# Optimization experiments

Hardware: AMD Instinct MI355X
Metric: run time of the kernel (lower is better)

The kernel has to match this reference:

```python
import jax, jax.numpy as jnp
import numpy as np

STATE = 1024

def setup_inputs() -> dict:
    key = jax.random.key(0)
    k1, k2, k3, k4, k5 = jax.random.split(key, 5)
    B, IN, S = 4096, 1024, STATE
    stdv = 1.0 / np.sqrt(S)
    return {
        "input": jax.random.normal(k1, (B, IN), jnp.float32),
        "old_h": jax.random.normal(k2, (B, S), jnp.float32),
        "old_cell": jax.random.normal(k3, (B, S), jnp.float32),
        "weights": jax.random.uniform(k4, (4 * S, IN + S), jnp.float32, -stdv, stdv),
        "bias": jax.random.uniform(k5, (4 * S,), jnp.float32, -stdv, stdv),
    }

def reference(input, old_h, old_cell, weights, bias):
    # Fused gate GEMM: X = [input, old_h] -> [B, IN+S]; gates -> [B, 4S]
    X = jnp.concatenate([input, old_h], axis=1)
    gates = X @ weights.T + bias
    f, i, o, g = jnp.split(gates, 4, axis=1)
    f = jax.nn.sigmoid(f)
    i = jax.nn.sigmoid(i)
    o = jax.nn.sigmoid(o)
    g = jnp.tanh(g)
    new_cell = f * old_cell + i * g
    new_h = o * jnp.tanh(new_cell)
    return new_h, new_cell
```

## Files before the change

kernel.cpp:

```cpp
#include <hip/hip_runtime.h>
#include <stdint.h>

#define NB   4096
#define KD   2048
#define ND   4096
#define SD   1024

#define BM   256
#define BN   256
#define BK   64
#define NKT  (KD / BK)

using f32x4  = __attribute__((ext_vector_type(4))) float;
using bf16x8 = __attribute__((ext_vector_type(8))) short;

typedef const __attribute__((address_space(1))) uint32_t* gas_u32;
typedef __attribute__((address_space(3))) uint32_t* las_u32;

__device__ __forceinline__ unsigned short f2bf(float f) {
    union { float f; uint32_t u; } c; c.f = f;
    uint32_t u = c.u;
    uint32_t r = (u + 0x7fffu + ((u >> 16) & 1u)) >> 16;
    return (unsigned short)r;
}

__device__ __forceinline__ void async_load16(const void* gsrc, void* ldst) {
    __builtin_amdgcn_global_load_lds((gas_u32)gsrc, (las_u32)ldst, 16, 0, 0);
}

__device__ __forceinline__ float frcp(float x) { return __builtin_amdgcn_rcpf(x); }
__device__ __forceinline__ float sigm(float x) { return frcp(1.f + __expf(-x)); }
__device__ __forceinline__ float tanh_fast(float x) {
    return 1.f - 2.f * frcp(1.f + __expf(2.f * x));
}

__global__ void pack_kernel(const float* __restrict__ input,
                            const float* __restrict__ old_h,
                            const float* __restrict__ weights,
                            const float* __restrict__ bias,
                            unsigned short* __restrict__ Xb,
                            unsigned short* __restrict__ Wb,
                            float* __restrict__ biasR) {
    const int XCH = NB * (KD / 4);
    const int WCH = ND * (KD / 4);
    const int BCH = ND / 4;
    const int total = XCH + WCH + BCH;
    for (int c = blockIdx.x * blockDim.x + threadIdx.x; c < total;
         c += gridDim.x * blockDim.x) {
        if (c < XCH) {
            int b  = c >> 9;
            int k  = (c & 511) << 2;
            const float* src = (k < 1024) ? (input + (size_t)b * 1024 + k)
                                          : (old_h + (size_t)b * 1024 + (k - 1024));
            float4 v = *reinterpret_cast<const float4*>(src);
            ushort4 o;
            o.x = f2bf(v.x); o.y = f2bf(v.y); o.z = f2bf(v.z); o.w = f2bf(v.w);
            *reinterpret_cast<ushort4*>(Xb + (size_t)b * KD + k) = o;
        } else if (c < XCH + WCH) {
            int cc = c - XCH;
            int n  = cc >> 9;
            int k  = (cc & 511) << 2;
            int srow = ((n >> 4) & 3) * SD + ((n >> 6) * 16 + (n & 15));
            float4 v = *reinterpret_cast<const float4*>(weights + (size_t)srow * KD + k);
            ushort4 o;
            o.x = f2bf(v.x); o.y = f2bf(v.y); o.z = f2bf(v.z); o.w = f2bf(v.w);
            *reinterpret_cast<ushort4*>(Wb + (size_t)n * KD + k) = o;
        } else {
            int n4 = (c - XCH - WCH) << 2;
            #pragma unroll
            for (int t = 0; t < 4; ++t) {
                int n = n4 + t;
                biasR[n] = bias[((n >> 4) & 3) * SD + ((n >> 6) * 16 + (n & 15))];
            }
        }
    }
}

#define SEG(DB, AB, HALF) (((((DB) * 2 + (AB)) * 2) + (HALF)) * 8192)

#define SBAR   __builtin_amdgcn_s_barrier()
#define SFENCE __builtin_amdgcn_sched_barrier(0)
#define ASM_LGKM0  asm volatile("s_waitcnt lgkmcnt(0)" ::: "memory")
#define ASM_VMCNT2 asm volatile("s_waitcnt vmcnt(2)" ::: "memory")
#define ASM_VMCNT4 asm volatile("s_waitcnt vmcnt(4)" ::: "memory")

__launch_bounds__(512, 2)
__global__ void lstm_gemm(const unsigned short* __restrict__ Xb,
                          const unsigned short* __restrict__ Wb,
                          const float* __restrict__ biasR,
                          const float* __restrict__ old_cell,
                          float* __restrict__ new_h,
                          float* __restrict__ new_cell) {
    __shared__ unsigned short lds[65536];

    const int tid  = threadIdx.x;
    const int lane = tid & 63;
    const int wid  = tid >> 6;
    const int wm   = wid >> 2;
    const int wn   = wid & 3;
    const int l15  = lane & 15;
    const int krow = lane >> 4;

    const int wg    = blockIdx.x;
    const int swz   = (wg & 7) * 32 + (wg >> 3);
    const int mblk  = swz >> 4;
    const int nblk  = swz & 15;
    const int rbase = mblk * BM;
    const int nbase = nblk * BN;

    const int c0 = tid, c1 = tid + 512;
    const int srow0 = c0 >> 3, sk0 = ((c0 & 7) ^ (srow0 & 7)) * 8;
    const int srow1 = c1 >> 3, sk1 = ((c1 & 7) ^ (srow1 & 7)) * 8;

    f32x4  acc[8][4] = {};
    bf16x8 a[4][2];
    bf16x8 bm[2][2];
    bf16x8 ba[2][2];

#define STAGE(PTR, TB, KT, DB, AB, HALF) do {                                   \
        async_load16((PTR) + (size_t)((TB) + (HALF) * 128 + srow0) * KD +       \
                         (KT) * BK + sk0,                                       \
                     lds + SEG(DB, AB, HALF) + c0 * 8);                         \
        async_load16((PTR) + (size_t)((TB) + (HALF) * 128 + srow1) * KD +       \
                         (KT) * BK + sk1,                                       \
                     lds + SEG(DB, AB, HALF) + c1 * 8);                         \
    } while (0)

#define LOAD_A(DB, MQ) do {                                                     \
        const unsigned short* base_ = lds + SEG(DB, 0, 0) + wm * 8192;          \
        _Pragma("unroll") for (int i_ = 0; i_ < 4; ++i_)                        \
        _Pragma("unroll") for (int kk_ = 0; kk_ < 2; ++kk_) {                   \
            int r_ = (MQ) * 64 + i_ * 16 + l15;                                 \
            int s_ = kk_ * 4 + krow;                                            \
            a[i_][kk_] = *reinterpret_cast<const bf16x8*>(                      \
                base_ + r_ * 64 + ((s_ ^ (r_ & 7)) * 8));                       \
        }                                                                       \
    } while (0)

#define LOAD_B_TO(DST, DB, NQ) do {                                             \
        const unsigned short* base_ = lds + SEG(DB, 1, 0) + (wn >> 1) * 8192;   \
        _Pragma("unroll") for (int j_ = 0; j_ < 2; ++j_)                        \
        _Pragma("unroll") for (int kk_ = 0; kk_ < 2; ++kk_) {                   \
            int r_ = (wn & 1) * 64 + ((NQ) * 2 + j_) * 16 + l15;                \
            int s_ = kk_ * 4 + krow;                                            \
            DST[j_][kk_] = *reinterpret_cast<const bf16x8*>(                    \
                base_ + r_ * 64 + ((s_ ^ (r_ & 7)) * 8));                       \
        }                                                                       \
    } while (0)

#define MMA_Q(MQ, NQH, BB) do {                                                 \
        _Pragma("unroll") for (int i_ = 0; i_ < 4; ++i_)                        \
        _Pragma("unroll") for (int j_ = 0; j_ < 2; ++j_)                        \
        _Pragma("unroll") for (int kk_ = 0; kk_ < 2; ++kk_)                     \
            acc[(MQ) * 4 + i_][(NQH) * 2 + j_] =                                \
                __builtin_amdgcn_mfma_f32_16x16x32_bf16(                        \
                    a[i_][kk_], BB[j_][kk_],                                    \
                    acc[(MQ) * 4 + i_][(NQH) * 2 + j_], 0, 0, 0);               \
    } while (0)

#define PH_HEAD   SFENCE; SBAR; ASM_LGKM0; SFENCE; __builtin_amdgcn_s_setprio(1)
#define PH_HEADV  SFENCE; ASM_VMCNT2; SBAR; ASM_LGKM0; SFENCE; __builtin_amdgcn_s_setprio(1)
#define PH_TAIL   __builtin_amdgcn_s_setprio(0); SFENCE; SBAR; SFENCE

    STAGE(Wb, nbase, 0, 0, 1, 0);
    STAGE(Wb, nbase, 0, 0, 1, 1);
    STAGE(Xb, rbase, 0, 0, 0, 0);
    STAGE(Xb, rbase, 0, 0, 0, 1);
    STAGE(Wb, nbase, 1, 1, 1, 0);
    STAGE(Wb, nbase, 1, 1, 1, 1);
    ASM_VMCNT4;
    SBAR; SFENCE;
    LOAD_B_TO(bm, 0, 0);
    LOAD_A(0, 0);

#define KBODY(TT, BUF) do {                                                     \
        const int kt1_ = ((TT) + 1) & (NKT - 1);                                \
        const int kt2_ = ((TT) + 2) & (NKT - 1);                                \
        STAGE(Xb, rbase, kt1_, (BUF) ^ 1, 0, 0);                                \
        PH_HEAD;  MMA_Q(0, 0, bm); LOAD_B_TO(ba, BUF, 1);      PH_TAIL;         \
        STAGE(Xb, rbase, kt1_, (BUF) ^ 1, 0, 1);                                \
        PH_HEAD;  MMA_Q(0, 1, ba); LOAD_A(BUF, 1);             PH_TAIL;         \
        STAGE(Wb, nbase, kt2_, BUF, 1, 0);                                      \
        PH_HEADV; MMA_Q(1, 0, bm); LOAD_B_TO(bm, (BUF) ^ 1, 0); PH_TAIL;        \
        STAGE(Wb, nbase, kt2_, BUF, 1, 1);                                      \
        PH_HEAD;  MMA_Q(1, 1, ba); LOAD_A((BUF) ^ 1, 0);       PH_TAIL;         \
    } while (0)

    for (int t = 0; t < NKT; t += 2) {
        KBODY(t, 0);
        KBODY(t + 1, 1);
    }

    const int s = (nblk * 4 + wn) * 16 + l15;
    float bg[4];
    #pragma unroll
    for (int jj = 0; jj < 4; ++jj)
        bg[jj] = biasR[nbase + wn * 64 + jj * 16 + l15];

    #pragma unroll
    for (int mi = 0; mi < 8; ++mi) {
        #pragma unroll
        for (int r = 0; r < 4; ++r) {
            const int row = rbase + wm * 128 + mi * 16 + krow * 4 + r;
            float fg = sigm(acc[mi][0][r] + bg[0]);
            float ig = sigm(acc[mi][1][r] + bg[1]);
            float og = sigm(acc[mi][2][r] + bg[2]);
            float gg = tanh_fast(acc[mi][3][r] + bg[3]);
            float oc = old_cell[(size_t)row * SD + s];
            float nc = fmaf(fg, oc, ig * gg);
            float nh = og * tanh_fast(nc);
            new_h[(size_t)row * SD + s]    = nh;
            new_cell[(size_t)row * SD + s] = nc;
        }
    }
}

extern "C" void kernel_launch(void* const* d_in, const int* in_sizes, int n_in,
                              void* d_out, int out_size, void* d_ws, size_t ws_size,
                              hipStream_t stream) {
    const float* input    = (const float*)d_in[0];
    const float* old_h    = (const float*)d_in[1];
    const float* old_cell = (const float*)d_in[2];
    const float* weights  = (const float*)d_in[3];
    const float* bias     = (const float*)d_in[4];

    unsigned short* Xb  = (unsigned short*)d_ws;
    unsigned short* Wb  = (unsigned short*)((char*)d_ws + (size_t)16777216);
    float*          bR  = (float*)((char*)d_ws + (size_t)33554432);

    float* out_h = (float*)d_out;
    float* out_c = out_h + (size_t)NB * SD;

    pack_kernel<<<2048, 256, 0, stream>>>(input, old_h, weights, bias, Xb, Wb, bR);
    lstm_gemm<<<(NB / BM) * (ND / BN), 512, 0, stream>>>(Xb, Wb, bR, old_cell,
                                                         out_h, out_c);
}
```

Baseline: 79.02 us.

## Restructure K-loop to load and consume LDS fragments per k-half phase

Replaces the register-prefetched fragment pipeline with per-phase loads that are used immediately. Each of the four phases now loads an A quarter for one k-half and, in the first two, a full B k-half, then issues 16 MFMAs. The explicit lgkmcnt waits and priority bumps are removed, and a single vmcnt wait is placed at the end of the body. This shrinks the fragment register footprint and simplifies synchronisation, but LDS read latency is no longer hidden behind the previous phase's MFMAs.

```diff
diff --git a/kernel.cpp b/kernel.cpp
--- a/kernel.cpp
+++ b/kernel.cpp
@@ -80,8 +80,6 @@
 
 #define SBAR   __builtin_amdgcn_s_barrier()
 #define SFENCE __builtin_amdgcn_sched_barrier(0)
-#define ASM_LGKM0  asm volatile("s_waitcnt lgkmcnt(0)" ::: "memory")
-#define ASM_VMCNT2 asm volatile("s_waitcnt vmcnt(2)" ::: "memory")
 #define ASM_VMCNT4 asm volatile("s_waitcnt vmcnt(4)" ::: "memory")
 
 __launch_bounds__(512, 2)
@@ -113,9 +111,9 @@
     const int srow1 = c1 >> 3, sk1 = ((c1 & 7) ^ (srow1 & 7)) * 8;
 
     f32x4  acc[8][4] = {};
-    bf16x8 a[4][2];
-    bf16x8 bm[2][2];
-    bf16x8 ba[2][2];
+    bf16x8 a[4];
+    bf16x8 bk0[4];
+    bf16x8 bk1[4];
 
 #define STAGE(PTR, TB, KT, DB, AB, HALF) do {                                   \
         async_load16((PTR) + (size_t)((TB) + (HALF) * 128 + srow0) * KD +       \
@@ -126,41 +124,33 @@
                      lds + SEG(DB, AB, HALF) + c1 * 8);                         \
     } while (0)
 
-#define LOAD_A(DB, MQ) do {                                                     \
+#define LOAD_A4(DB, MQ, KK) do {                                                \
         const unsigned short* base_ = lds + SEG(DB, 0, 0) + wm * 8192;          \
-        _Pragma("unroll") for (int i_ = 0; i_ < 4; ++i_)                        \
-        _Pragma("unroll") for (int kk_ = 0; kk_ < 2; ++kk_) {                   \
+        _Pragma("unroll") for (int i_ = 0; i_ < 4; ++i_) {                      \
             int r_ = (MQ) * 64 + i_ * 16 + l15;                                 \
-            int s_ = kk_ * 4 + krow;                                            \
-            a[i_][kk_] = *reinterpret_cast<const bf16x8*>(                      \
+            int s_ = (KK) * 4 + krow;                                           \
+            a[i_] = *reinterpret_cast<const bf16x8*>(                           \
                 base_ + r_ * 64 + ((s_ ^ (r_ & 7)) * 8));                       \
         }                                                                       \
     } while (0)
 
-#define LOAD_B_TO(DST, DB, NQ) do {                                             \
+#define LOAD_B4(DST, DB, KK) do {                                               \
         const unsigned short* base_ = lds + SEG(DB, 1, 0) + (wn >> 1) * 8192;   \
-        _Pragma("unroll") for (int j_ = 0; j_ < 2; ++j_)                        \
-        _Pragma("unroll") for (int kk_ = 0; kk_ < 2; ++kk_) {                   \
-            int r_ = (wn & 1) * 64 + ((NQ) * 2 + j_) * 16 + l15;                \
-            int s_ = kk_ * 4 + krow;                                            \
-            DST[j_][kk_] = *reinterpret_cast<const bf16x8*>(                    \
+        _Pragma("unroll") for (int j_ = 0; j_ < 4; ++j_) {                      \
+            int r_ = (wn & 1) * 64 + j_ * 16 + l15;                             \
+            int s_ = (KK) * 4 + krow;                                           \
+            DST[j_] = *reinterpret_cast<const bf16x8*>(                         \
                 base_ + r_ * 64 + ((s_ ^ (r_ & 7)) * 8));                       \
         }                                                                       \
     } while (0)
 
-#define MMA_Q(MQ, NQH, BB) do {                                                 \
+#define MMA16(MQ, BB) do {                                                      \
         _Pragma("unroll") for (int i_ = 0; i_ < 4; ++i_)                        \
-        _Pragma("unroll") for (int j_ = 0; j_ < 2; ++j_)                        \
-        _Pragma("unroll") for (int kk_ = 0; kk_ < 2; ++kk_)                     \
-            acc[(MQ) * 4 + i_][(NQH) * 2 + j_] =                                \
+        _Pragma("unroll") for (int j_ = 0; j_ < 4; ++j_)                        \
+            acc[(MQ) * 4 + i_][j_] =                                            \
                 __builtin_amdgcn_mfma_f32_16x16x32_bf16(                        \
-                    a[i_][kk_], BB[j_][kk_],                                    \
-                    acc[(MQ) * 4 + i_][(NQH) * 2 + j_], 0, 0, 0);               \
-    } while (0)
-
-#define PH_HEAD   SFENCE; SBAR; ASM_LGKM0; SFENCE; __builtin_amdgcn_s_setprio(1)
-#define PH_HEADV  SFENCE; ASM_VMCNT2; SBAR; ASM_LGKM0; SFENCE; __builtin_amdgcn_s_setprio(1)
-#define PH_TAIL   __builtin_amdgcn_s_setprio(0); SFENCE; SBAR; SFENCE
+                    a[i_], BB[j_], acc[(MQ) * 4 + i_][j_], 0, 0, 0);            \
+    } while (0)
 
     STAGE(Wb, nbase, 0, 0, 1, 0);
     STAGE(Wb, nbase, 0, 0, 1, 1);
@@ -169,21 +159,35 @@
     STAGE(Wb, nbase, 1, 1, 1, 0);
     STAGE(Wb, nbase, 1, 1, 1, 1);
     ASM_VMCNT4;
-    SBAR; SFENCE;
-    LOAD_B_TO(bm, 0, 0);
-    LOAD_A(0, 0);
+    SBAR;
+    SFENCE;
 
 #define KBODY(TT, BUF) do {                                                     \
         const int kt1_ = ((TT) + 1) & (NKT - 1);                                \
         const int kt2_ = ((TT) + 2) & (NKT - 1);                                \
+                      \
         STAGE(Xb, rbase, kt1_, (BUF) ^ 1, 0, 0);                                \
-        PH_HEAD;  MMA_Q(0, 0, bm); LOAD_B_TO(ba, BUF, 1);      PH_TAIL;         \
+        LOAD_A4(BUF, 0, 0);                                                     \
+        LOAD_B4(bk0, BUF, 0);                                                   \
+        MMA16(0, bk0);                                                          \
+        SBAR; SFENCE;                                                           \
+                      \
         STAGE(Xb, rbase, kt1_, (BUF) ^ 1, 0, 1);                                \
-        PH_HEAD;  MMA_Q(0, 1, ba); LOAD_A(BUF, 1);             PH_TAIL;         \
+        LOAD_A4(BUF, 0, 1);                                                     \
+        LOAD_B4(bk1, BUF, 1);                                                   \
+        MMA16(0, bk1);                                                          \
+        SBAR; SFENCE;                                                           \
+               \
         STAGE(Wb, nbase, kt2_, BUF, 1, 0);                                      \
-        PH_HEADV; MMA_Q(1, 0, bm); LOAD_B_TO(bm, (BUF) ^ 1, 0); PH_TAIL;        \
+        LOAD_A4(BUF, 1, 0);                                                     \
+        MMA16(1, bk0);                                                          \
+        SBAR; SFENCE;                                                           \
+              \
         STAGE(Wb, nbase, kt2_, BUF, 1, 1);                                      \
-        PH_HEAD;  MMA_Q(1, 1, ba); LOAD_A((BUF) ^ 1, 0);       PH_TAIL;         \
+        LOAD_A4(BUF, 1, 1);                                                     \
+        MMA16(1, bk1);                                                          \
+        ASM_VMCNT4;                                                             \
+        SBAR; SFENCE;                                                           \
     } while (0)
 
     for (int t = 0; t < NKT; t += 2) {
```

Result: no change. 77.80 us (-1.5%).

## Restructure GEMM main loop with precomputed LDS addresses and reordered load/MMA phases

Applied to the files above, without the earlier changes.

Rewrites the pipelined bf16 GEMM main loop. LDS read addresses are precomputed per lane as byte offsets, and global source pointers are hoisted. The LDS layout is changed into separate A and B regions. The phase schedule now issues LDS fragment loads before the MMAs, with partial lgkmcnt waits and explicit double-buffered B registers (b0/b1). The goal is to cut address arithmetic and improve overlap of LDS reads, async global loads and MFMA work. In exchange, it drops the sched_barrier fences and the memory clobbers on the lgkm waits, which risks compiler reordering and correctness or schedule problems.

```diff
diff --git a/kernel.cpp b/kernel.cpp
--- a/kernel.cpp
+++ b/kernel.cpp
@@ -76,13 +76,15 @@
     }
 }
 
-#define SEG(DB, AB, HALF) (((((DB) * 2 + (AB)) * 2) + (HALF)) * 8192)
+#define LDS_A(DB, HALF) (((DB) * 2 + (HALF)) * 16384)
+#define LDS_B(DB, HALF) (65536 + ((DB) * 2 + (HALF)) * 16384)
 
 #define SBAR   __builtin_amdgcn_s_barrier()
-#define SFENCE __builtin_amdgcn_sched_barrier(0)
-#define ASM_LGKM0  asm volatile("s_waitcnt lgkmcnt(0)" ::: "memory")
-#define ASM_VMCNT2 asm volatile("s_waitcnt vmcnt(2)" ::: "memory")
-#define ASM_VMCNT4 asm volatile("s_waitcnt vmcnt(4)" ::: "memory")
+#define LGKM8  asm volatile("s_waitcnt lgkmcnt(8)")
+#define LGKM0  asm volatile("s_waitcnt lgkmcnt(0)")
+#define VMC4   asm volatile("s_waitcnt vmcnt(4)" ::: "memory")
+#define PRIO1  __builtin_amdgcn_s_setprio(1)
+#define PRIO0  __builtin_amdgcn_s_setprio(0)
 
 __launch_bounds__(512, 2)
 __global__ void lstm_gemm(const unsigned short* __restrict__ Xb,
@@ -92,6 +94,7 @@
                           float* __restrict__ new_h,
                           float* __restrict__ new_cell) {
     __shared__ unsigned short lds[65536];
+    char* const ldsc = (char*)lds;
 
     const int tid  = threadIdx.x;
     const int lane = tid & 63;
@@ -108,43 +111,57 @@
     const int rbase = mblk * BM;
     const int nbase = nblk * BN;
 
+    const int lx   = l15 & 7;
+    const int lrow = l15 * 128;
+    const int sw0  = ((krow)     ^ lx) * 16;
+    const int sw1  = ((krow + 4) ^ lx) * 16;
+    const int vA00 = LDS_A(0, 0) + wm * 16384 + lrow + sw0;
+    const int vA01 = LDS_A(0, 0) + wm * 16384 + lrow + sw1;
+    const int vA10 = LDS_A(1, 0) + wm * 16384 + lrow + sw0;
+    const int vA11 = LDS_A(1, 0) + wm * 16384 + lrow + sw1;
+    const int bpan = (wn >> 1) * 16384 + (wn & 1) * 8192;
+    const int vB00 = LDS_B(0, 0) + bpan + lrow + sw0;
+    const int vB01 = LDS_B(0, 0) + bpan + lrow + sw1;
+    const int vB10 = LDS_B(1, 0) + bpan + lrow + sw0;
+    const int vB11 = LDS_B(1, 0) + bpan + lrow + sw1;
+
     const int c0 = tid, c1 = tid + 512;
     const int srow0 = c0 >> 3, sk0 = ((c0 & 7) ^ (srow0 & 7)) * 8;
     const int srow1 = c1 >> 3, sk1 = ((c1 & 7) ^ (srow1 & 7)) * 8;
+    const unsigned short* const pX0 = Xb + (size_t)(rbase + srow0) * KD + sk0;
+    const unsigned short* const pX1 = Xb + (size_t)(rbase + srow1) * KD + sk1;
+    const unsigned short* const pW0 = Wb + (size_t)(nbase + srow0) * KD + sk0;
+    const unsigned short* const pW1 = Wb + (size_t)(nbase + srow1) * KD + sk1;
+    const int ldst0 = tid * 16, ldst1 = tid * 16 + 8192;
 
     f32x4  acc[8][4] = {};
     bf16x8 a[4][2];
-    bf16x8 bm[2][2];
-    bf16x8 ba[2][2];
-
-#define STAGE(PTR, TB, KT, DB, AB, HALF) do {                                   \
-        async_load16((PTR) + (size_t)((TB) + (HALF) * 128 + srow0) * KD +       \
-                         (KT) * BK + sk0,                                       \
-                     lds + SEG(DB, AB, HALF) + c0 * 8);                         \
-        async_load16((PTR) + (size_t)((TB) + (HALF) * 128 + srow1) * KD +       \
-                         (KT) * BK + sk1,                                       \
-                     lds + SEG(DB, AB, HALF) + c1 * 8);                         \
-    } while (0)
-
-#define LOAD_A(DB, MQ) do {                                                     \
-        const unsigned short* base_ = lds + SEG(DB, 0, 0) + wm * 8192;          \
-        _Pragma("unroll") for (int i_ = 0; i_ < 4; ++i_)                        \
-        _Pragma("unroll") for (int kk_ = 0; kk_ < 2; ++kk_) {                   \
-            int r_ = (MQ) * 64 + i_ * 16 + l15;                                 \
-            int s_ = kk_ * 4 + krow;                                            \
-            a[i_][kk_] = *reinterpret_cast<const bf16x8*>(                      \
-                base_ + r_ * 64 + ((s_ ^ (r_ & 7)) * 8));                       \
+    bf16x8 b0[2][2];
+    bf16x8 b1[2][2];
+
+#define STAGE_X(KT, DB, HALF) do {                                              \
+        async_load16(pX0 + (HALF) * 128 * KD + (KT) * BK, ldsc + LDS_A(DB, HALF) + ldst0); \
+        async_load16(pX1 + (HALF) * 128 * KD + (KT) * BK, ldsc + LDS_A(DB, HALF) + ldst1); \
+    } while (0)
+#define STAGE_W(KT, DB, HALF) do {                                              \
+        async_load16(pW0 + (HALF) * 128 * KD + (KT) * BK, ldsc + LDS_B(DB, HALF) + ldst0); \
+        async_load16(pW1 + (HALF) * 128 * KD + (KT) * BK, ldsc + LDS_B(DB, HALF) + ldst1); \
+    } while (0)
+
+#define LOAD_A(V0, V1, MQ) do {                                                 \
+        _Pragma("unroll") for (int i_ = 0; i_ < 4; ++i_) {                      \
+            a[i_][0] = *reinterpret_cast<const bf16x8*>(                        \
+                ldsc + (V0) + (MQ) * 8192 + i_ * 2048);                         \
+            a[i_][1] = *reinterpret_cast<const bf16x8*>(                        \
+                ldsc + (V1) + (MQ) * 8192 + i_ * 2048);                         \
         }                                                                       \
     } while (0)
-
-#define LOAD_B_TO(DST, DB, NQ) do {                                             \
-        const unsigned short* base_ = lds + SEG(DB, 1, 0) + (wn >> 1) * 8192;   \
-        _Pragma("unroll") for (int j_ = 0; j_ < 2; ++j_)                        \
-        _Pragma("unroll") for (int kk_ = 0; kk_ < 2; ++kk_) {                   \
-            int r_ = (wn & 1) * 64 + ((NQ) * 2 + j_) * 16 + l15;                \
-            int s_ = kk_ * 4 + krow;                                            \
-            DST[j_][kk_] = *reinterpret_cast<const bf16x8*>(                    \
-                base_ + r_ * 64 + ((s_ ^ (r_ & 7)) * 8));                       \
+#define LOAD_B(DST, V0, V1, NQ) do {                                            \
+        _Pragma("unroll") for (int j_ = 0; j_ < 2; ++j_) {                      \
+            DST[j_][0] = *reinterpret_cast<const bf16x8*>(                      \
+                ldsc + (V0) + (NQ) * 4096 + j_ * 2048);                         \
+            DST[j_][1] = *reinterpret_cast<const bf16x8*>(                      \
+                ldsc + (V1) + (NQ) * 4096 + j_ * 2048);                         \
         }                                                                       \
     } while (0)
 
@@ -158,37 +175,46 @@
                     acc[(MQ) * 4 + i_][(NQH) * 2 + j_], 0, 0, 0);               \
     } while (0)
 
-#define PH_HEAD   SFENCE; SBAR; ASM_LGKM0; SFENCE; __builtin_amdgcn_s_setprio(1)
-#define PH_HEADV  SFENCE; ASM_VMCNT2; SBAR; ASM_LGKM0; SFENCE; __builtin_amdgcn_s_setprio(1)
-#define PH_TAIL   __builtin_amdgcn_s_setprio(0); SFENCE; SBAR; SFENCE
-
-    STAGE(Wb, nbase, 0, 0, 1, 0);
-    STAGE(Wb, nbase, 0, 0, 1, 1);
-    STAGE(Xb, rbase, 0, 0, 0, 0);
-    STAGE(Xb, rbase, 0, 0, 0, 1);
-    STAGE(Wb, nbase, 1, 1, 1, 0);
-    STAGE(Wb, nbase, 1, 1, 1, 1);
-    ASM_VMCNT4;
-    SBAR; SFENCE;
-    LOAD_B_TO(bm, 0, 0);
-    LOAD_A(0, 0);
-
-#define KBODY(TT, BUF) do {                                                     \
-        const int kt1_ = ((TT) + 1) & (NKT - 1);                                \
-        const int kt2_ = ((TT) + 2) & (NKT - 1);                                \
-        STAGE(Xb, rbase, kt1_, (BUF) ^ 1, 0, 0);                                \
-        PH_HEAD;  MMA_Q(0, 0, bm); LOAD_B_TO(ba, BUF, 1);      PH_TAIL;         \
-        STAGE(Xb, rbase, kt1_, (BUF) ^ 1, 0, 1);                                \
-        PH_HEAD;  MMA_Q(0, 1, ba); LOAD_A(BUF, 1);             PH_TAIL;         \
-        STAGE(Wb, nbase, kt2_, BUF, 1, 0);                                      \
-        PH_HEADV; MMA_Q(1, 0, bm); LOAD_B_TO(bm, (BUF) ^ 1, 0); PH_TAIL;        \
-        STAGE(Wb, nbase, kt2_, BUF, 1, 1);                                      \
-        PH_HEAD;  MMA_Q(1, 1, ba); LOAD_A((BUF) ^ 1, 0);       PH_TAIL;         \
-    } while (0)
+    STAGE_W(0, 0, 0);
+    STAGE_W(0, 0, 1);
+    STAGE_X(0, 0, 0);
+    STAGE_X(0, 0, 1);
+    STAGE_W(1, 1, 0);
+    STAGE_W(1, 1, 1);
+    VMC4;
+    SBAR;
 
     for (int t = 0; t < NKT; t += 2) {
-        KBODY(t, 0);
-        KBODY(t + 1, 1);
+        const int kt1 = t + 1;
+        const int kt2 = (t + 2) & (NKT - 1);
+        const int kt3 = (t + 3) & (NKT - 1);
+
+        LOAD_A(vA00, vA01, 0);
+        LOAD_B(b0, vB00, vB01, 0);
+        STAGE_X(kt1, 1, 0);
+        LGKM8;
+        SBAR; LGKM0; PRIO1; MMA_Q(0, 0, b0); PRIO0; SBAR;
+        LOAD_B(b1, vB00, vB01, 1);
+        STAGE_X(kt1, 1, 1);
+        SBAR; LGKM0; PRIO1; MMA_Q(0, 1, b1); PRIO0; SBAR;
+        LOAD_A(vA00, vA01, 1);
+        STAGE_W(kt2, 0, 0);
+        SBAR; LGKM0; PRIO1; MMA_Q(1, 0, b0); PRIO0; SBAR;
+        STAGE_W(kt2, 0, 1);
+        SBAR; LGKM0; PRIO1; MMA_Q(1, 1, b1); PRIO0; VMC4; SBAR;
+        LOAD_A(vA10, vA11, 0);
+        LOAD_B(b0, vB10, vB11, 0);
+        STAGE_X(kt2, 0, 0);
+        LGKM8;
+        SBAR; LGKM0; PRIO1; MMA_Q(0, 0, b0); PRIO0; SBAR;
+        LOAD_B(b1, vB10, vB11, 1);
+        STAGE_X(kt2, 0, 1);
+        SBAR; LGKM0; PRIO1; MMA_Q(0, 1, b1); PRIO0; SBAR;
+        LOAD_A(vA10, vA11, 1);
+        STAGE_W(kt3, 1, 0);
+        SBAR; LGKM0; PRIO1; MMA_Q(1, 0, b0); PRIO0; SBAR;
+        STAGE_W(kt3, 1, 1);
+        SBAR; LGKM0; PRIO1; MMA_Q(1, 1, b1); PRIO0; VMC4; SBAR;
     }
 
     const int s = (nblk * 4 + wn) * 16 + l15;
```

New measurement: 80.63 us. +2.0%, slower.
